# Kernel tuning notes

Measured on AMD Instinct MI355X. Metric: run time of the kernel, lower is better.

## Reference

```python
import jax, jax.numpy as jnp
import numpy as np

B, T, D, H = 512, 128, 512, 512
FORGET_BIAS = 1.0

def setup_inputs() -> dict:
    key = jax.random.key(0)
    k1, k2 = jax.random.split(key)
    x = jax.random.normal(k1, (B, T, D), dtype=jnp.float32)
    # BasicLSTMCell kernel: [D+H, 4H], gate order i, j, f, o
    W = jax.random.normal(k2, (D + H, 4 * H), dtype=jnp.float32) * 0.05
    b = jnp.zeros((4 * H,), dtype=jnp.float32)
    return {"x": x, "W": W, "b": b}

def reference(x, W, b):
    # x: [B, T, D]; W: [D+H, 4H]; b: [4H]
    Bv, Tv, Dv = x.shape
    Hv = W.shape[1] // 4
    c0 = jnp.zeros((Bv, Hv), dtype=x.dtype)
    h0 = jnp.zeros((Bv, Hv), dtype=x.dtype)

    def step(carry, xt):
        c, h = carry
        z = jnp.concatenate([xt, h], axis=-1) @ W + b  # [B, 4H]
        i, j, f, o = jnp.split(z, 4, axis=-1)
        c_new = c * jax.nn.sigmoid(f + FORGET_BIAS) + jax.nn.sigmoid(i) * jnp.tanh(j)
        h_new = jnp.tanh(c_new) * jax.nn.sigmoid(o)
        return (c_new, h_new), None

    xs = jnp.swapaxes(x, 0, 1)  # [T, B, D]
    (c_T, h_T), _ = jax.lax.scan(step, (c0, h0), xs)
    # static_rnn returns all outputs; module returns outputs[-1] == h_T
    return h_T
```

## Files before the change

### kernel.cpp

```cpp
#include <hip/hip_runtime.h>


#define Tt  128
#define Dd  512
#define Hh  512

typedef _Float16 half8 __attribute__((ext_vector_type(8)));
typedef _Float16 half4 __attribute__((ext_vector_type(4)));
typedef float    f32x4 __attribute__((ext_vector_type(4)));
typedef float    f32x2 __attribute__((ext_vector_type(2)));
typedef unsigned long long u64;

#define MF(a,b,c) __builtin_amdgcn_mfma_f32_16x16x32_f16(a,b,c,0,0,0)

#define Z_OFF   0
#define H_OFF   16384
#define R_OFF   49152
#define X_OFF   81920
#define SMEM_SZ 147456

__device__ __forceinline__ float sigm(float v) { return 1.0f / (1.0f + __expf(-v)); }
__device__ __forceinline__ float tanhfast(float v) {
    float e = __expf(-2.0f * fabsf(v));
    float r = (1.0f - e) / (1.0f + e);
    return (v < 0.0f) ? -r : r;
}
__device__ __forceinline__ half8 mk16(u64 a, u64 b) {
    half4 x = __builtin_bit_cast(half4, a), y = __builtin_bit_cast(half4, b);
    half8 r;
    r[0] = x[0]; r[1] = x[1]; r[2] = x[2]; r[3] = x[3];
    r[4] = y[0]; r[5] = y[1]; r[6] = y[2]; r[7] = y[3];
    return r;
}

__global__ __launch_bounds__(256) void pack_kernel(const float* __restrict__ W,
                                                   _Float16* __restrict__ Wxp,
                                                   _Float16* __restrict__ Whp) {
    __shared__ _Float16 Tl[512 * 32];
    const int bid = blockIdx.x, tid = threadIdx.x;
    const int which = bid >> 6;
    const int f = bid & 63, ct = f >> 2, wv = f & 3;
    const int koff = which * 512;
    const int ncol0 = wv * Hh + ct * 32;

#pragma unroll
    for (int p = 0; p < 16; ++p) {
        int row = p * 32 + (tid >> 3);
        int c4  = (tid & 7) * 4;
        float4 v = *reinterpret_cast<const float4*>(W + (size_t)(koff + row) * 2048 + ncol0 + c4);
        Tl[row * 32 + c4 + 0] = (_Float16)v.x;
        Tl[row * 32 + c4 + 1] = (_Float16)v.y;
        Tl[row * 32 + c4 + 2] = (_Float16)v.z;
        Tl[row * 32 + c4 + 3] = (_Float16)v.w;
    }
    __syncthreads();

    _Float16* dst = (which ? Whp : Wxp) + (size_t)f * 16384;
#pragma unroll
    for (int i = 0; i < 8; ++i) {
        int gi  = tid * 8 + i;
        int hn  = gi >> 10;
        int kc  = (gi >> 6) & 15;
        int ln  = gi & 63;
        int l15 = ln & 15, l16 = ln >> 4;
        half8 v;
#pragma unroll
        for (int j = 0; j < 8; ++j)
            v[j] = Tl[(kc * 32 + l16 * 8 + j) * 32 + hn * 16 + l15];
        *reinterpret_cast<half8*>(dst + (size_t)gi * 8) = v;
    }
}

__global__ __launch_bounds__(256) void xhalf_kernel(const float* __restrict__ xf,
                                                    _Float16* __restrict__ xh) {
    const size_t N = (size_t)512 * Tt * Dd;
    size_t stride = (size_t)gridDim.x * 256 * 8;
    for (size_t base = ((size_t)blockIdx.x * 256 + threadIdx.x) * 8; base < N; base += stride) {
        float4 a = *reinterpret_cast<const float4*>(xf + base);
        float4 b = *reinterpret_cast<const float4*>(xf + base + 4);
        half8 v;
        v[0] = (_Float16)a.x; v[1] = (_Float16)a.y; v[2] = (_Float16)a.z; v[3] = (_Float16)a.w;
        v[4] = (_Float16)b.x; v[5] = (_Float16)b.y; v[6] = (_Float16)b.z; v[7] = (_Float16)b.w;
        *reinterpret_cast<half8*>(xh + base) = v;
    }
}

__global__ __launch_bounds__(512, 2) void lstm_all(
    const float* __restrict__ xf, const _Float16* __restrict__ xh, int usexh,
    const _Float16* __restrict__ Wxp, const _Float16* __restrict__ Whp,
    const float* __restrict__ bias, _Float16* __restrict__ h0,
    _Float16* __restrict__ h1, unsigned int* __restrict__ flags,
    float* __restrict__ out) {

    __shared__ __align__(16) char smem[SMEM_SZ];

    const int tid = threadIdx.x, lane = tid & 63;
    const int wv8 = tid >> 6;
    const int g8  = wv8 >> 1;
    const int nh  = wv8 & 1;
    const int l15 = lane & 15, l16 = lane >> 4;
    const int bid = blockIdx.x;
    const int grp = bid & 15;
    const int rt = (bid & 7) * 2 + ((bid >> 3) & 1);
    const int ct = bid >> 4;

    half8 wxr[16], whr[16];
    {
        const half8* wxs = reinterpret_cast<const half8*>(Wxp)
                           + (size_t)(ct * 4 + g8) * 2048 + nh * 1024;
        const half8* whs = reinterpret_cast<const half8*>(Whp)
                           + (size_t)(ct * 4 + g8) * 2048 + nh * 1024;
#pragma unroll
        for (int kc = 0; kc < 16; ++kc) {
            wxr[kc] = wxs[kc * 64 + lane];
            whr[kc] = whs[kc * 64 + lane];
        }
    }

    const float biasv = bias[g8 * Hh + ct * 32 + nh * 16 + l15] + (g8 == 2 ? 1.0f : 0.0f);

    const int srow = tid >> 4, sl16 = tid & 15;
    const int erow = tid >> 4, ecol2 = (tid & 15) * 2;
    const int sswz = (srow & 7) << 4;
    float creg[2] = {0.f, 0.f};

    f32x4 accG0, accG1;

    auto xload = [&](int g, half8 xl[4]) {
        if (usexh) {
            const _Float16* xr = xh + ((size_t)(rt * 32 + srow) * Tt + g) * Dd + sl16 * 8;
#pragma unroll
            for (int c = 0; c < 4; ++c)
                xl[c] = *reinterpret_cast<const half8*>(xr + c * 128);
        } else {
            const float* xr = xf + ((size_t)(rt * 32 + srow) * Tt + g) * Dd + sl16 * 8;
#pragma unroll
            for (int c = 0; c < 4; ++c) {
                float4 p0 = *reinterpret_cast<const float4*>(xr + c * 128);
                float4 p1 = *reinterpret_cast<const float4*>(xr + c * 128 + 4);
                half8 v;
                v[0] = (_Float16)p0.x; v[1] = (_Float16)p0.y;
                v[2] = (_Float16)p0.z; v[3] = (_Float16)p0.w;
                v[4] = (_Float16)p1.x; v[5] = (_Float16)p1.y;
                v[6] = (_Float16)p1.z; v[7] = (_Float16)p1.w;
                xl[c] = v;
            }
        }
    };
    auto xwrite = [&](int xb, half8 xl[4]) {
        char* xbase = smem + X_OFF + xb * 32768 + srow * 1024;
#pragma unroll
        for (int c = 0; c < 4; ++c)
            *reinterpret_cast<half8*>(xbase + ((c * 256 + sl16 * 16) ^ sswz)) = xl[c];
    };

    auto gemm_range = [&](int xb, int k0, int k1) {
        const char* xbase = smem + X_OFF + xb * 32768;
#pragma unroll
        for (int kc = k0; kc < k1; ++kc) {
            int go = kc * 64 + l16 * 16;
            half8 a0 = *reinterpret_cast<const half8*>(
                xbase + l15 * 1024 + (go ^ ((l15 & 7) << 4)));
            half8 a1 = *reinterpret_cast<const half8*>(
                xbase + (16 + l15) * 1024 + (go ^ ((l15 & 7) << 4)));
            accG0 = MF(a0, wxr[kc], accG0);
            accG1 = MF(a1, wxr[kc], accG1);
        }
    };

    auto ring_write = [&](int slot) {
        half8 z;
#pragma unroll
        for (int r = 0; r < 4; ++r) {
            z[r]     = (_Float16)accG0[r];
            z[4 + r] = (_Float16)accG1[r];
        }
        *reinterpret_cast<half8*>(smem + R_OFF + slot * 8192 + wv8 * 1024 + lane * 16) = z;
    };

#pragma unroll 1
    for (int p = 0; p < 4; ++p) {
        { half8 xl[4]; xload(p, xl); xwrite(p & 1, xl); }
        __syncthreads();
        accG0 = f32x4{biasv, biasv, biasv, biasv}; accG1 = accG0;
        gemm_range(p & 1, 0, 16);
        ring_write(p);
        __syncthreads();
    }
    { half8 xl[4]; xload(4, xl); xwrite(0, xl); }
    __syncthreads();

#pragma unroll 1
    for (int t = 0; t < Tt; ++t) {
        const int xb = t & 1;
        const int slot = t & 3;
        const bool do_g  = (t + 4) < Tt;
        const bool do_g2 = (t + 5) < Tt;
        const _Float16* hin = (t & 1) ? h1 : h0;
        _Float16* hout      = (t & 1) ? h0 : h1;

        half8 xl[4];
        if (do_g2) xload(t + 5, xl);

        if (do_g) {
            accG0 = f32x4{biasv, biasv, biasv, biasv}; accG1 = accG0;
            gemm_range(xb, 0, 8);
        }

        f32x4 acc0, acc1;
        {
            half8 z = *reinterpret_cast<const half8*>(
                smem + R_OFF + slot * 8192 + wv8 * 1024 + lane * 16);
#pragma unroll
            for (int r = 0; r < 4; ++r) { acc0[r] = (float)z[r]; acc1[r] = (float)z[4 + r]; }
        }

        if (tid < 16) {
            while (__hip_atomic_load(&flags[((unsigned)grp + 16u * (unsigned)tid) * 16u],
                                     __ATOMIC_RELAXED, __HIP_MEMORY_SCOPE_AGENT)
                   < (unsigned)t)
                __builtin_amdgcn_s_sleep(1);
        }
        __syncthreads();

        const u64* hq = reinterpret_cast<const u64*>(
                            hin + (size_t)(rt * 32 + srow) * Hh) + sl16 * 2;
        u64 hr[8];
#pragma unroll
        for (int c = 0; c < 4; ++c) {
            hr[2 * c]     = __hip_atomic_load(hq + c * 32,     __ATOMIC_RELAXED,
                                              __HIP_MEMORY_SCOPE_AGENT);
            hr[2 * c + 1] = __hip_atomic_load(hq + c * 32 + 1, __ATOMIC_RELAXED,
                                              __HIP_MEMORY_SCOPE_AGENT);
        }

        if (do_g) {
            gemm_range(xb, 8, 16);
            ring_write(slot);
        }

        {
            char* hb = smem + H_OFF + srow * 1024;
#pragma unroll
            for (int c = 0; c < 4; ++c)
                *reinterpret_cast<half8*>(hb + ((c * 256 + sl16 * 16) ^ sswz)) =
                    mk16(hr[2 * c], hr[2 * c + 1]);
        }
        __syncthreads();

#pragma unroll
        for (int kc = 0; kc < 16; ++kc) {
            int go = kc * 64 + l16 * 16;
            half8 a0 = *reinterpret_cast<const half8*>(
                smem + H_OFF + l15 * 1024 + (go ^ ((l15 & 7) << 4)));
            half8 a1 = *reinterpret_cast<const half8*>(
                smem + H_OFF + (16 + l15) * 1024 + (go ^ ((l15 & 7) << 4)));
            acc0 = MF(a0, whr[kc], acc0);
            acc1 = MF(a1, whr[kc], acc1);
        }

#pragma unroll
        for (int reg = 0; reg < 4; ++reg) {
            int zr = l16 * 4 + reg;
            int cb = ((nh * 16 + l15) * 4) ^ ((zr & 7) << 4);
            *reinterpret_cast<float*>(smem + Z_OFF + (g8 * 32 + zr) * 128 + cb)      = acc0[reg];
            *reinterpret_cast<float*>(smem + Z_OFF + (g8 * 32 + 16 + zr) * 128 + cb) = acc1[reg];
        }
        __syncthreads();

        float hv[2];
        {
            int swz = (ecol2 * 4) ^ ((erow & 7) << 4);
            f32x2 vi = *reinterpret_cast<const f32x2*>(smem + Z_OFF + (0 * 32 + erow) * 128 + swz);
            f32x2 vj = *reinterpret_cast<const f32x2*>(smem + Z_OFF + (1 * 32 + erow) * 128 + swz);
            f32x2 vf = *reinterpret_cast<const f32x2*>(smem + Z_OFF + (2 * 32 + erow) * 128 + swz);
            f32x2 vo = *reinterpret_cast<const f32x2*>(smem + Z_OFF + (3 * 32 + erow) * 128 + swz);
#pragma unroll
            for (int q = 0; q < 2; ++q) {
                float cn = creg[q] * sigm(vf[q]) + sigm(vi[q]) * tanhfast(vj[q]);
                creg[q] = cn;
                hv[q] = tanhfast(cn) * sigm(vo[q]);
            }
        }
        {
            size_t off = (size_t)(rt * 32 + erow) * Hh + ct * 32 + ecol2;
            unsigned hraw = (unsigned)__builtin_bit_cast(unsigned short, (_Float16)hv[0])
                          | ((unsigned)__builtin_bit_cast(unsigned short, (_Float16)hv[1]) << 16);
            __hip_atomic_store(reinterpret_cast<unsigned*>(hout) + (off >> 1), hraw,
                               __ATOMIC_RELAXED, __HIP_MEMORY_SCOPE_AGENT);
            if (t == Tt - 1) {
                f32x2 fo; fo[0] = hv[0]; fo[1] = hv[1];
                *reinterpret_cast<f32x2*>(out + off) = fo;
            }
        }

        if (do_g2) xwrite((t + 1) & 1, xl);

        __syncthreads();
        if (t < Tt - 1 && tid == 0)
            __hip_atomic_store(&flags[bid * 16], (unsigned)(t + 1),
                               __ATOMIC_RELAXED, __HIP_MEMORY_SCOPE_AGENT);
    }
}

extern "C" void kernel_launch(void* const* d_in, const int* in_sizes, int n_in,
                              void* d_out, int out_size, void* d_ws, size_t ws_size,
                              hipStream_t stream) {
    const float* x  = (const float*)d_in[0];
    const float* W  = (const float*)d_in[1];
    const float* bb = (const float*)d_in[2];
    float* out = (float*)d_out;

    char* ws = (char*)d_ws;
    _Float16* Wxp = (_Float16*)ws;
    _Float16* Whp = (_Float16*)(ws + (2u << 20));
    _Float16* h0  = (_Float16*)(ws + (4u << 20));
    _Float16* h1  = (_Float16*)(ws + (4u << 20) + (512u << 10));
    unsigned int* flags = (unsigned int*)(ws + (5u << 20));
    _Float16* xh = (_Float16*)(ws + (6u << 20));

    const size_t xh_bytes = (size_t)512 * Tt * Dd * sizeof(_Float16);
    int usexh = (ws_size >= (size_t)(6u << 20) + xh_bytes) ? 1 : 0;

    hipMemsetAsync(h0, 0, (size_t)512 * Hh * sizeof(_Float16), stream);
    hipMemsetAsync((void*)flags, 0, 16384, stream);
    pack_kernel<<<128, 256, 0, stream>>>(W, Wxp, Whp);
    if (usexh) xhalf_kernel<<<4096, 256, 0, stream>>>(x, xh);
    lstm_all<<<256, 512, 0, stream>>>(x, xh, usexh, Wxp, Whp, bb, h0, h1, flags, out);
}
```

Before: 514.1 us.

## Map blocks to row groups by XCD and reorder flag wait before x-GEMM

Each block reads its XCC id from a hardware register and publishes it to a table. When all blocks have registered and the layout is balanced (8 XCDs with 32 blocks each), blocks are renumbered so that each row group sharing h data sits on one XCD. In that mode h is read with plain sc0 vector loads instead of agent-scope atomics. The flag wait and h load are moved ahead of the input-projection GEMM, so the load latency overlaps that GEMM, which is no longer split into two halves. The change adds a grid-wide startup handshake and relies on all 256 blocks being resident at once. Its correctness depends on per-XCD L2 coherence for the sc0 loads.

New measurement: 599.7 us. 1.17x slower.

```diff
diff --git a/kernel.cpp b/kernel.cpp
--- a/kernel.cpp
+++ b/kernel.cpp
@@ -90,7 +90,7 @@
     const _Float16* __restrict__ Wxp, const _Float16* __restrict__ Whp,
     const float* __restrict__ bias, _Float16* __restrict__ h0,
     _Float16* __restrict__ h1, unsigned int* __restrict__ flags,
-    float* __restrict__ out) {
+    unsigned int* __restrict__ xcdtab, float* __restrict__ out) {
 
     __shared__ __align__(16) char smem[SMEM_SZ];
 
@@ -100,9 +100,41 @@
     const int nh  = wv8 & 1;
     const int l15 = lane & 15, l16 = lane >> 4;
     const int bid = blockIdx.x;
-    const int grp = bid & 15;
-    const int rt = (bid & 7) * 2 + ((bid >> 3) & 1);
-    const int ct = bid >> 4;
+
+    bool fast;
+    int grp, rt, ct;
+    {
+        const unsigned myxcc =
+            (unsigned)__builtin_amdgcn_s_getreg(20 | (0 << 6) | (3 << 11)) & 0xFu;
+        if (tid == 0)
+            __hip_atomic_store(&xcdtab[bid], 0x100u | myxcc,
+                               __ATOMIC_RELAXED, __HIP_MEMORY_SCOPE_AGENT);
+        if (tid < 256) {
+            unsigned v;
+            while (!((v = __hip_atomic_load(&xcdtab[tid], __ATOMIC_RELAXED,
+                                            __HIP_MEMORY_SCOPE_AGENT)) & 0x100u))
+                __builtin_amdgcn_s_sleep(2);
+            ((int*)smem)[tid] = (int)(v & 15u);
+        }
+        __syncthreads();
+        int cnt[16];
+#pragma unroll
+        for (int i = 0; i < 16; ++i) cnt[i] = 0;
+        int pos = 0;
+        for (int i = 0; i < 256; ++i) {
+            int xv = ((int*)smem)[i];
+            cnt[xv]++;
+            pos += (xv < (int)myxcc) || (xv == (int)myxcc && i < bid);
+        }
+        int nz = 0; bool all32 = true;
+        for (int v = 0; v < 16; ++v)
+            if (cnt[v]) { nz++; if (cnt[v] != 32) all32 = false; }
+        fast = (nz == 8) && all32;
+        __syncthreads();
+        if (fast) { grp = pos >> 4; rt = grp; ct = pos & 15; }
+        else      { grp = bid & 15; rt = (bid & 7) * 2 + ((bid >> 3) & 1); ct = bid >> 4; }
+    }
+    unsigned* const myflag = flags + (grp * 16 + ct) * 16;
 
     half8 wxr[16], whr[16];
     {
@@ -202,9 +234,37 @@
         half8 xl[4];
         if (do_g2) xload(t + 5, xl);
 
-        if (do_g) {
-            accG0 = f32x4{biasv, biasv, biasv, biasv}; accG1 = accG0;
-            gemm_range(xb, 0, 8);
+        if (tid < 16) {
+            while (__hip_atomic_load(flags + (grp * 16 + tid) * 16,
+                                     __ATOMIC_RELAXED, __HIP_MEMORY_SCOPE_AGENT)
+                   < (unsigned)t)
+                __builtin_amdgcn_s_sleep(1);
+        }
+        __syncthreads();
+
+        f32x4 gq0, gq1, gq2, gq3;
+        u64 hr[8];
+        if (fast) {
+            const char* hb = reinterpret_cast<const char*>(hin)
+                             + (size_t)(rt * 32 + srow) * 1024 + sl16 * 16;
+            asm volatile(
+                "global_load_dwordx4 %0, %4, off sc0\n\t"
+                "global_load_dwordx4 %1, %5, off sc0\n\t"
+                "global_load_dwordx4 %2, %6, off sc0\n\t"
+                "global_load_dwordx4 %3, %7, off sc0"
+                : "=&v"(gq0), "=&v"(gq1), "=&v"(gq2), "=&v"(gq3)
+                : "v"(hb), "v"(hb + 256), "v"(hb + 512), "v"(hb + 768)
+                : "memory");
+        } else {
+            const u64* hq = reinterpret_cast<const u64*>(
+                                hin + (size_t)(rt * 32 + srow) * Hh) + sl16 * 2;
+#pragma unroll
+            for (int c = 0; c < 4; ++c) {
+                hr[2 * c]     = __hip_atomic_load(hq + c * 32,     __ATOMIC_RELAXED,
+                                                  __HIP_MEMORY_SCOPE_AGENT);
+                hr[2 * c + 1] = __hip_atomic_load(hq + c * 32 + 1, __ATOMIC_RELAXED,
+                                                  __HIP_MEMORY_SCOPE_AGENT);
+            }
         }
 
         f32x4 acc0, acc1;
@@ -215,36 +275,31 @@
             for (int r = 0; r < 4; ++r) { acc0[r] = (float)z[r]; acc1[r] = (float)z[4 + r]; }
         }
 
-        if (tid < 16) {
-            while (__hip_atomic_load(&flags[((unsigned)grp + 16u * (unsigned)tid) * 16u],
-                                     __ATOMIC_RELAXED, __HIP_MEMORY_SCOPE_AGENT)
-                   < (unsigned)t)
-                __builtin_amdgcn_s_sleep(1);
-        }
-        __syncthreads();
-
-        const u64* hq = reinterpret_cast<const u64*>(
-                            hin + (size_t)(rt * 32 + srow) * Hh) + sl16 * 2;
-        u64 hr[8];
-#pragma unroll
-        for (int c = 0; c < 4; ++c) {
-            hr[2 * c]     = __hip_atomic_load(hq + c * 32,     __ATOMIC_RELAXED,
-                                              __HIP_MEMORY_SCOPE_AGENT);
-            hr[2 * c + 1] = __hip_atomic_load(hq + c * 32 + 1, __ATOMIC_RELAXED,
-                                              __HIP_MEMORY_SCOPE_AGENT);
-        }
-
         if (do_g) {
-            gemm_range(xb, 8, 16);
+            accG0 = f32x4{biasv, biasv, biasv, biasv}; accG1 = accG0;
+            gemm_range(xb, 0, 16);
             ring_write(slot);
+        }
+
+        half8 hv4[4];
+        if (fast) {
+            asm volatile("s_waitcnt vmcnt(0)"
+                         : "+v"(gq0), "+v"(gq1), "+v"(gq2), "+v"(gq3) :: "memory");
+            __builtin_amdgcn_sched_barrier(0);
+            hv4[0] = __builtin_bit_cast(half8, gq0);
+            hv4[1] = __builtin_bit_cast(half8, gq1);
+            hv4[2] = __builtin_bit_cast(half8, gq2);
+            hv4[3] = __builtin_bit_cast(half8, gq3);
+        } else {
+#pragma unroll
+            for (int c = 0; c < 4; ++c) hv4[c] = mk16(hr[2 * c], hr[2 * c + 1]);
         }
 
         {
             char* hb = smem + H_OFF + srow * 1024;
 #pragma unroll
             for (int c = 0; c < 4; ++c)
-                *reinterpret_cast<half8*>(hb + ((c * 256 + sl16 * 16) ^ sswz)) =
-                    mk16(hr[2 * c], hr[2 * c + 1]);
+                *reinterpret_cast<half8*>(hb + ((c * 256 + sl16 * 16) ^ sswz)) = hv4[c];
         }
         __syncthreads();
 
@@ -298,7 +353,7 @@
 
         __syncthreads();
         if (t < Tt - 1 && tid == 0)
-            __hip_atomic_store(&flags[bid * 16], (unsigned)(t + 1),
+            __hip_atomic_store(myflag, (unsigned)(t + 1),
                                __ATOMIC_RELAXED, __HIP_MEMORY_SCOPE_AGENT);
     }
 }
@@ -316,15 +371,16 @@
     _Float16* Whp = (_Float16*)(ws + (2u << 20));
     _Float16* h0  = (_Float16*)(ws + (4u << 20));
     _Float16* h1  = (_Float16*)(ws + (4u << 20) + (512u << 10));
-    unsigned int* flags = (unsigned int*)(ws + (5u << 20));
+    unsigned int* flags  = (unsigned int*)(ws + (5u << 20));
+    unsigned int* xcdtab = (unsigned int*)(ws + (5u << 20) + 16384);
     _Float16* xh = (_Float16*)(ws + (6u << 20));
 
     const size_t xh_bytes = (size_t)512 * Tt * Dd * sizeof(_Float16);
     int usexh = (ws_size >= (size_t)(6u << 20) + xh_bytes) ? 1 : 0;
 
     hipMemsetAsync(h0, 0, (size_t)512 * Hh * sizeof(_Float16), stream);
-    hipMemsetAsync((void*)flags, 0, 16384, stream);
+    hipMemsetAsync((void*)flags, 0, 16384 + 2048, stream);
     pack_kernel<<<128, 256, 0, stream>>>(W, Wxp, Whp);
     if (usexh) xhalf_kernel<<<4096, 256, 0, stream>>>(x, xh);
-    lstm_all<<<256, 512, 0, stream>>>(x, xh, usexh, Wxp, Whp, bb, h0, h1, flags, out);
-}
+    lstm_all<<<256, 512, 0, stream>>>(x, xh, usexh, Wxp, Whp, bb, h0, h1, flags, xcdtab, out);
+}
```
